# Optimization experiments

Measured on AMD Instinct MI355X. Metric: run time of the kernel, lower is better.

Reference implementation:

```python
import jax, jax.numpy as jnp
import numpy as np

B, S, D, H = 4, 1024, 1024, 16
HD = D // H  # head dim = 64
SCALE = 1.0 / float(np.sqrt(HD))
W_INIT = 0.02


def setup_inputs() -> dict:
    key = jax.random.key(0)
    ks = jax.random.split(key, 8)
    f = lambda k, shape: jax.random.normal(k, shape, dtype=jnp.float32)
    return {
        "q": f(ks[0], (B, S, D)),
        "k": f(ks[1], (B, S, D)),
        "v": f(ks[2], (B, S, D)),
        "Wq": f(ks[3], (D, D)) * W_INIT, "bq": jnp.zeros((D,), jnp.float32),
        "Wk": f(ks[4], (D, D)) * W_INIT, "bk": jnp.zeros((D,), jnp.float32),
        "Wv": f(ks[5], (D, D)) * W_INIT, "bv": jnp.zeros((D,), jnp.float32),
        "Wo": f(ks[6], (D, D)) * W_INIT, "bo": jnp.zeros((D,), jnp.float32),
    }


def _split_heads(x):
    # [B, S, D] -> [B, H, S, HD]
    return x.reshape(B, S, H, HD).transpose(0, 2, 1, 3)


def reference(q, k, v, Wq, bq, Wk, bk, Wv, bv, Wo, bo):
    # linear input projections (torch Linear: x @ W.T + b)
    qh = _split_heads(q @ Wq.T + bq) * SCALE
    kh = _split_heads(k @ Wk.T + bk)
    vh = _split_heads(v @ Wv.T + bv)
    # scaled dot-product attention, full score matrix as in the source
    scores = jnp.einsum("bhqd,bhkd->bhqk", qh, kh)  # [B,H,S,S]
    weights = jax.nn.softmax(scores, axis=-1)
    ctx = jnp.einsum("bhqk,bhkd->bhqd", weights, vh)  # [B,H,S,HD]
    ctx = ctx.transpose(0, 2, 1, 3).reshape(B, S, D)
    # output projection (dropout=0, activation=None -> identity)
    return ctx @ Wo.T + bo
```

## Files before the change

kernel.cpp:

```cpp
#include <hip/hip_runtime.h>
#include <hip/hip_bf16.h>

typedef __attribute__((ext_vector_type(8))) short short8;
typedef __attribute__((ext_vector_type(4))) float f32x4;

static __device__ __forceinline__ short f2bf(float x) {
    __hip_bfloat16 h(x);
    return __builtin_bit_cast(short, h);
}

static __device__ __forceinline__ void gload16(const void* g, void* l) {
    auto* gp = reinterpret_cast<const __attribute__((address_space(1))) unsigned*>(
        reinterpret_cast<uintptr_t>(g));
    auto* lp = reinterpret_cast<__attribute__((address_space(3))) unsigned*>(
        reinterpret_cast<uintptr_t>(l));
    __builtin_amdgcn_global_load_lds(gp, lp, 16, 0, 0);
}

template <int CTRL>
static __device__ __forceinline__ float dppf(float v) {
    return __builtin_bit_cast(float,
        __builtin_amdgcn_mov_dpp(__builtin_bit_cast(int, v), CTRL, 0xF, 0xF, true));
}
static __device__ __forceinline__ float red16_max(float v) {
    v = fmaxf(v, dppf<0xB1>(v));
    v = fmaxf(v, dppf<0x4E>(v));
    v = fmaxf(v, dppf<0x141>(v));
    v = fmaxf(v, dppf<0x140>(v));
    return v;
}
static __device__ __forceinline__ float red16_sum(float v) {
    v += dppf<0xB1>(v);
    v += dppf<0x4E>(v);
    v += dppf<0x141>(v);
    v += dppf<0x140>(v);
    return v;
}

__global__ __launch_bounds__(256) void convert_w3(
    const float* __restrict__ Wq, const float* __restrict__ Wk,
    const float* __restrict__ Wv, short* __restrict__ dst)
{
    const size_t e = ((size_t)blockIdx.x * 256 + threadIdx.x) * 8;
    const int seg = (int)(e >> 20);
    const float* src = (seg == 0) ? Wq : (seg == 1) ? Wk : Wv;
    const size_t off = e & 1048575;
    float4 f0 = *(const float4*)(src + off);
    float4 f1 = *(const float4*)(src + off + 4);
    short8 o;
    o[0] = f2bf(f0.x); o[1] = f2bf(f0.y); o[2] = f2bf(f0.z); o[3] = f2bf(f0.w);
    o[4] = f2bf(f1.x); o[5] = f2bf(f1.y); o[6] = f2bf(f1.z); o[7] = f2bf(f1.w);
    *(short8*)(dst + e) = o;
}

__global__ __launch_bounds__(256) void convert_w1(
    const float* __restrict__ W, short* __restrict__ dst)
{
    const size_t e = ((size_t)blockIdx.x * 256 + threadIdx.x) * 8;
    float4 f0 = *(const float4*)(W + e);
    float4 f1 = *(const float4*)(W + e + 4);
    short8 o;
    o[0] = f2bf(f0.x); o[1] = f2bf(f0.y); o[2] = f2bf(f0.z); o[3] = f2bf(f0.w);
    o[4] = f2bf(f1.x); o[5] = f2bf(f1.y); o[6] = f2bf(f1.z); o[7] = f2bf(f1.w);
    *(short8*)(dst + e) = o;
}

__global__ __launch_bounds__(256) void proj_qkv_kernel(
    const float* __restrict__ q, const float* __restrict__ k, const float* __restrict__ v,
    const short* __restrict__ wbf,
    const float* __restrict__ bq, const float* __restrict__ bk, const float* __restrict__ bv,
    short* __restrict__ qh, short* __restrict__ kh, short* __restrict__ vt)
{
    const int z = blockIdx.z;
    const float* A    = (z == 0) ? q  : (z == 1) ? k  : v;
    const short* W    = wbf + (size_t)z * 1048576;
    const float* bias = (z == 0) ? bq : (z == 1) ? bk : bv;

    __shared__ __align__(16) short As[2][128 * 32];
    __shared__ __align__(16) short Bs[2][128 * 32];

    const int tid = threadIdx.x;
    const int lane = tid & 63;
    const int w = tid >> 6;
    const int wr = w >> 1, wc = w & 1;
    const int row0 = blockIdx.x * 128;
    const int col0 = blockIdx.y * 128;
    const int fr = lane & 15;
    const int g = lane >> 4;
    const int fk = g * 8;

    const int brow = lane >> 2;
    const int bch  = (lane & 3) * 8;
    const int arow = tid >> 2;
    const int ach  = (tid & 3) * 8;

    f32x4 acc[4][4] = {};
    float4 pfA[2][2];

    #pragma unroll
    for (int i = 0; i < 2; ++i) {
        const int r0 = w * 32 + i * 16;
        gload16(W + (size_t)(col0 + r0 + brow) * 1024 + bch, &Bs[0][r0 * 32]);
    }
    #pragma unroll
    for (int p = 0; p < 2; ++p) {
        const int r = p * 64 + arow;
        const float* s = A + (size_t)(row0 + r) * 1024 + ach;
        float4 f0 = *(const float4*)s, f1 = *(const float4*)(s + 4);
        short8 o;
        o[0] = f2bf(f0.x); o[1] = f2bf(f0.y); o[2] = f2bf(f0.z); o[3] = f2bf(f0.w);
        o[4] = f2bf(f1.x); o[5] = f2bf(f1.y); o[6] = f2bf(f1.z); o[7] = f2bf(f1.w);
        *(short8*)&As[0][r * 32 + ach] = o;
    }
    __syncthreads();

    for (int t = 0; t < 32; ++t) {
        const int cur = t & 1, nxt = cur ^ 1;
        if (t < 31) {
            const int k1 = (t + 1) * 32;
            #pragma unroll
            for (int i = 0; i < 2; ++i) {
                const int r0 = w * 32 + i * 16;
                gload16(W + (size_t)(col0 + r0 + brow) * 1024 + k1 + bch, &Bs[nxt][r0 * 32]);
            }
            #pragma unroll
            for (int p = 0; p < 2; ++p) {
                const float* s = A + (size_t)(row0 + p * 64 + arow) * 1024 + k1 + ach;
                pfA[p][0] = *(const float4*)s;
                pfA[p][1] = *(const float4*)(s + 4);
            }
        }
        short8 aF[4], bF[4];
        #pragma unroll
        for (int m = 0; m < 4; ++m) aF[m] = *(const short8*)&As[cur][(wr * 64 + m * 16 + fr) * 32 + fk];
        #pragma unroll
        for (int n = 0; n < 4; ++n) bF[n] = *(const short8*)&Bs[cur][(wc * 64 + n * 16 + fr) * 32 + fk];
        if (z == 2) {
            #pragma unroll
            for (int m = 0; m < 4; ++m)
                #pragma unroll
                for (int n = 0; n < 4; ++n)
                    acc[m][n] = __builtin_amdgcn_mfma_f32_16x16x32_bf16(bF[n], aF[m], acc[m][n], 0, 0, 0);
        } else {
            #pragma unroll
            for (int m = 0; m < 4; ++m)
                #pragma unroll
                for (int n = 0; n < 4; ++n)
                    acc[m][n] = __builtin_amdgcn_mfma_f32_16x16x32_bf16(aF[m], bF[n], acc[m][n], 0, 0, 0);
        }
        if (t < 31) {
            #pragma unroll
            for (int p = 0; p < 2; ++p) {
                float4 f0 = pfA[p][0], f1 = pfA[p][1];
                short8 o;
                o[0] = f2bf(f0.x); o[1] = f2bf(f0.y); o[2] = f2bf(f0.z); o[3] = f2bf(f0.w);
                o[4] = f2bf(f1.x); o[5] = f2bf(f1.y); o[6] = f2bf(f1.z); o[7] = f2bf(f1.w);
                *(short8*)&As[nxt][(p * 64 + arow) * 32 + ach] = o;
            }
        }
        __syncthreads();
    }

    const int gg = lane >> 4;
    if (z == 2) {
        #pragma unroll
        for (int n = 0; n < 4; ++n) {
            #pragma unroll
            for (int i = 0; i < 4; ++i) {
                const int c = col0 + wc * 64 + n * 16 + gg * 4 + i;
                const int h = c >> 6, hd = c & 63;
                const float bb = bias[c];
                #pragma unroll
                for (int m = 0; m < 4; ++m) {
                    const int r = row0 + wr * 64 + m * 16 + fr;
                    const int b = r >> 10, s = r & 1023;
                    vt[(((size_t)(b * 16 + h) * 64 + hd) << 10) + s] = f2bf(acc[m][n][i] + bb);
                }
            }
        }
    } else {
        short* out = (z == 0) ? qh : kh;
        const float scale = (z == 0) ? 0.125f : 1.0f;
        #pragma unroll
        for (int n = 0; n < 4; ++n) {
            const int c = col0 + wc * 64 + n * 16 + fr;
            const int h = c >> 6, hd = c & 63;
            const float bb = bias[c];
            #pragma unroll
            for (int m = 0; m < 4; ++m) {
                #pragma unroll
                for (int i = 0; i < 4; ++i) {
                    const int r = row0 + wr * 64 + m * 16 + gg * 4 + i;
                    const int b = r >> 10, s = r & 1023;
                    out[(((size_t)(b * 16 + h) * 1024 + s) << 6) + hd] =
                        f2bf((acc[m][n][i] + bb) * scale);
                }
            }
        }
    }
}

__global__ __launch_bounds__(256) void proj_o_kernel(
    const short* __restrict__ ctx, const short* __restrict__ wo,
    const float* __restrict__ bo, float* __restrict__ out)
{
    __shared__ __align__(16) short As[2][128 * 32];
    __shared__ __align__(16) short Bs[2][64 * 32];

    const int tid = threadIdx.x;
    const int lane = tid & 63;
    const int w = tid >> 6;
    const int row0 = blockIdx.x * 128;
    const int col0 = blockIdx.y * 64;
    const int fr = lane & 15;
    const int g = lane >> 4;
    const int fk = g * 8;
    const int brow = lane >> 2;
    const int bch  = (lane & 3) * 8;

    f32x4 acc[2][4] = {};

    #pragma unroll
    for (int i = 0; i < 2; ++i) {
        const int r0 = w * 32 + i * 16;
        gload16(ctx + (size_t)(row0 + r0 + brow) * 1024 + bch, &As[0][r0 * 32]);
    }
    gload16(wo + (size_t)(col0 + w * 16 + brow) * 1024 + bch, &Bs[0][w * 16 * 32]);
    __syncthreads();

    for (int t = 0; t < 32; ++t) {
        const int cur = t & 1, nxt = cur ^ 1;
        if (t < 31) {
            const int k1 = (t + 1) * 32;
            #pragma unroll
            for (int i = 0; i < 2; ++i) {
                const int r0 = w * 32 + i * 16;
                gload16(ctx + (size_t)(row0 + r0 + brow) * 1024 + k1 + bch, &As[nxt][r0 * 32]);
            }
            gload16(wo + (size_t)(col0 + w * 16 + brow) * 1024 + k1 + bch, &Bs[nxt][w * 16 * 32]);
        }
        short8 aF[2], bF[4];
        #pragma unroll
        for (int m = 0; m < 2; ++m)
            aF[m] = *(const short8*)&As[cur][(w * 32 + m * 16 + fr) * 32 + fk];
        #pragma unroll
        for (int n = 0; n < 4; ++n)
            bF[n] = *(const short8*)&Bs[cur][(n * 16 + fr) * 32 + fk];
        #pragma unroll
        for (int m = 0; m < 2; ++m)
            #pragma unroll
            for (int n = 0; n < 4; ++n)
                acc[m][n] = __builtin_amdgcn_mfma_f32_16x16x32_bf16(aF[m], bF[n], acc[m][n], 0, 0, 0);
        __syncthreads();
    }

    #pragma unroll
    for (int n = 0; n < 4; ++n) {
        const int c = col0 + n * 16 + fr;
        const float bb = bo[c];
        #pragma unroll
        for (int m = 0; m < 2; ++m) {
            #pragma unroll
            for (int i = 0; i < 4; ++i) {
                const int r = row0 + w * 32 + m * 16 + g * 4 + i;
                out[(size_t)r * 1024 + c] = acc[m][n][i] + bb;
            }
        }
    }
}

__global__ __launch_bounds__(256) void attn_kernel(
    const short* __restrict__ qh, const short* __restrict__ kh,
    const short* __restrict__ vt, short* __restrict__ ctx)
{
    const int d = blockIdx.x;
    const int xcd = d & 7;
    const int s2 = d >> 3;
    const int bh = xcd * 8 + (s2 >> 3);
    const int qb = s2 & 7;
    const int b = bh >> 4, h = bh & 15;
    const int q0 = qb * 128;
    const short* Qh  = qh + (size_t)bh * 65536;
    const short* Kh  = kh + (size_t)bh * 65536;
    const short* Vth = vt + (size_t)bh * 65536;

    __shared__ __align__(16) short Ks[2][64 * 64];
    __shared__ __align__(16) short Vs[2][64 * 64];
    __shared__ __align__(16) short Pb[4][2][16 * 68];

    const int tid = threadIdx.x;
    const int lane = tid & 63;
    const int w = tid >> 6;
    const int fr = lane & 15;
    const int g = lane >> 4;
    const int fk = g * 8;
    const int srow = lane >> 3;
    const int sch  = ((lane & 7) ^ srow) * 8;

    short8 qF[2][2];
    #pragma unroll
    for (int m = 0; m < 2; ++m)
        #pragma unroll
        for (int j = 0; j < 2; ++j)
            qF[m][j] = *(const short8*)(Qh + (q0 + w * 32 + m * 16 + fr) * 64 + j * 32 + fk);

    float mi[2][4], li[2][4];
    f32x4 o[2][4] = {};
    #pragma unroll
    for (int m = 0; m < 2; ++m)
        #pragma unroll
        for (int i = 0; i < 4; ++i) { mi[m][i] = -3.0e38f; li[m][i] = 0.0f; }

    #pragma unroll
    for (int i = 0; i < 2; ++i) {
        const int r0 = w * 16 + i * 8;
        gload16(Kh + (size_t)(r0 + srow) * 64 + sch, &Ks[0][r0 * 64]);
        gload16(Vth + (size_t)(r0 + srow) * 1024 + sch, &Vs[0][r0 * 64]);
    }
    __syncthreads();

    for (int kt = 0; kt < 16; ++kt) {
        const int cur = kt & 1;
        if (kt < 15) {
            const int kv1 = (kt + 1) * 64;
            #pragma unroll
            for (int i = 0; i < 2; ++i) {
                const int r0 = w * 16 + i * 8;
                gload16(Kh + (size_t)(kv1 + r0 + srow) * 64 + sch, &Ks[cur ^ 1][r0 * 64]);
                gload16(Vth + (size_t)(r0 + srow) * 1024 + kv1 + sch, &Vs[cur ^ 1][r0 * 64]);
            }
        }

        f32x4 sc[2][4] = {};
        #pragma unroll
        for (int n = 0; n < 4; ++n) {
            const int r = n * 16 + fr;
            #pragma unroll
            for (int j = 0; j < 2; ++j) {
                short8 kF = *(const short8*)&Ks[cur][r * 64 + (((j * 4 + g) ^ (fr & 7)) * 8)];
                #pragma unroll
                for (int m = 0; m < 2; ++m)
                    sc[m][n] = __builtin_amdgcn_mfma_f32_16x16x32_bf16(qF[m][j], kF, sc[m][n], 0, 0, 0);
            }
        }

        #pragma unroll
        for (int m = 0; m < 2; ++m) {
            #pragma unroll
            for (int i = 0; i < 4; ++i) {
                float t0 = fmaxf(fmaxf(sc[m][0][i], sc[m][1][i]),
                                 fmaxf(sc[m][2][i], sc[m][3][i]));
                const float tm = red16_max(t0);
                const float mn = fmaxf(mi[m][i], tm);
                const float al = __expf(mi[m][i] - mn);
                mi[m][i] = mn;
                float s0 = 0.0f;
                #pragma unroll
                for (int n = 0; n < 4; ++n) {
                    const float pv = __expf(sc[m][n][i] - mn);
                    s0 += pv;
                    Pb[w][m][(g * 4 + i) * 68 + n * 16 + fr] = f2bf(pv);
                }
                li[m][i] = li[m][i] * al + red16_sum(s0);
                #pragma unroll
                for (int n = 0; n < 4; ++n) o[m][n][i] *= al;
            }
        }

        #pragma unroll
        for (int half = 0; half < 2; ++half) {
            short8 pF[2];
            #pragma unroll
            for (int m = 0; m < 2; ++m)
                pF[m] = *(const short8*)&Pb[w][m][fr * 68 + half * 32 + fk];
            #pragma unroll
            for (int n = 0; n < 4; ++n) {
                short8 vF = *(const short8*)&Vs[cur][(n * 16 + fr) * 64 + (((half * 4 + g) ^ (fr & 7)) * 8)];
                #pragma unroll
                for (int m = 0; m < 2; ++m)
                    o[m][n] = __builtin_amdgcn_mfma_f32_16x16x32_bf16(pF[m], vF, o[m][n], 0, 0, 0);
            }
        }
        __syncthreads();
    }

    #pragma unroll
    for (int m = 0; m < 2; ++m) {
        float inv[4];
        #pragma unroll
        for (int i = 0; i < 4; ++i) inv[i] = 1.0f / li[m][i];
        #pragma unroll
        for (int n = 0; n < 4; ++n)
            #pragma unroll
            for (int i = 0; i < 4; ++i) {
                const int s = q0 + w * 32 + m * 16 + g * 4 + i;
                ctx[(size_t)(b * 1024 + s) * 1024 + h * 64 + n * 16 + fr] = f2bf(o[m][n][i] * inv[i]);
            }
    }
}

extern "C" void kernel_launch(void* const* d_in, const int* in_sizes, int n_in,
                              void* d_out, int out_size, void* d_ws, size_t ws_size,
                              hipStream_t stream) {
    const float* q  = (const float*)d_in[0];
    const float* k  = (const float*)d_in[1];
    const float* v  = (const float*)d_in[2];
    const float* Wq = (const float*)d_in[3];
    const float* bq = (const float*)d_in[4];
    const float* Wk = (const float*)d_in[5];
    const float* bk = (const float*)d_in[6];
    const float* Wv = (const float*)d_in[7];
    const float* bv = (const float*)d_in[8];
    const float* Wo = (const float*)d_in[9];
    const float* bo = (const float*)d_in[10];

    char* ws = (char*)d_ws;
    const size_t SZ = (size_t)4096 * 1024 * 2;
    short* qh  = (short*)(ws);
    short* kh  = (short*)(ws + SZ);
    short* vt  = (short*)(ws + 2 * SZ);
    short* ctx = (short*)(ws + 3 * SZ);
    short* wscratch = (short*)d_out;

    convert_w3<<<1536, 256, 0, stream>>>(Wq, Wk, Wv, wscratch);
    proj_qkv_kernel<<<dim3(32, 8, 3), 256, 0, stream>>>(
        q, k, v, wscratch, bq, bk, bv, qh, kh, vt);
    attn_kernel<<<512, 256, 0, stream>>>(qh, kh, vt, ctx);
    convert_w1<<<512, 256, 0, stream>>>(Wo, qh);
    proj_o_kernel<<<dim3(32, 16), 256, 0, stream>>>(ctx, qh, bo, (float*)d_out);
}
```

Before: 249.1 us.

## Pre-convert activations to bf16, use 64-wide K tiles, enlarge output tiles, add setprio

Input activations and all four weights are converted to bf16 in one kernel, and the QKV projection loads bf16 tiles straight into LDS with global_load_lds instead of converting fp32 in registers. Both projection GEMMs now use single-buffered 128x64 K tiles with two MFMA sub-steps, replacing double-buffered 32-wide tiles. The output projection moves to 128x128 tiles, and the attention MFMA sections get s_setprio hints. The extra conversion pass writes and rereads the activations, and dropping double buffering exposes load latency.

```diff
diff --git a/kernel.cpp b/kernel.cpp
--- a/kernel.cpp
+++ b/kernel.cpp
@@ -37,47 +37,49 @@
     return v;
 }
 
-__global__ __launch_bounds__(256) void convert_w3(
+__global__ __launch_bounds__(256) void convert_all(
+    const float* __restrict__ q, const float* __restrict__ k, const float* __restrict__ v,
     const float* __restrict__ Wq, const float* __restrict__ Wk,
-    const float* __restrict__ Wv, short* __restrict__ dst)
+    const float* __restrict__ Wv, const float* __restrict__ Wo,
+    short* __restrict__ abf_q, short* __restrict__ abf_k, short* __restrict__ abf_v,
+    short* __restrict__ wbf)
 {
-    const size_t e = ((size_t)blockIdx.x * 256 + threadIdx.x) * 8;
-    const int seg = (int)(e >> 20);
-    const float* src = (seg == 0) ? Wq : (seg == 1) ? Wk : Wv;
-    const size_t off = e & 1048575;
+    const int blk = blockIdx.x;
+    const float* src;
+    short* dst;
+    size_t off;
+    if (blk < 6144) {
+        const int seg = blk >> 11;
+        src = (seg == 0) ? q : (seg == 1) ? k : v;
+        dst = (seg == 0) ? abf_q : (seg == 1) ? abf_k : abf_v;
+        off = ((size_t)(blk & 2047) * 256 + threadIdx.x) * 8;
+    } else {
+        const int wseg = (blk - 6144) >> 9;
+        src = (wseg == 0) ? Wq : (wseg == 1) ? Wk : (wseg == 2) ? Wv : Wo;
+        dst = wbf + (size_t)wseg * 1048576;
+        off = ((size_t)((blk - 6144) & 511) * 256 + threadIdx.x) * 8;
+    }
     float4 f0 = *(const float4*)(src + off);
     float4 f1 = *(const float4*)(src + off + 4);
     short8 o;
     o[0] = f2bf(f0.x); o[1] = f2bf(f0.y); o[2] = f2bf(f0.z); o[3] = f2bf(f0.w);
     o[4] = f2bf(f1.x); o[5] = f2bf(f1.y); o[6] = f2bf(f1.z); o[7] = f2bf(f1.w);
-    *(short8*)(dst + e) = o;
-}
-
-__global__ __launch_bounds__(256) void convert_w1(
-    const float* __restrict__ W, short* __restrict__ dst)
-{
-    const size_t e = ((size_t)blockIdx.x * 256 + threadIdx.x) * 8;
-    float4 f0 = *(const float4*)(W + e);
-    float4 f1 = *(const float4*)(W + e + 4);
-    short8 o;
-    o[0] = f2bf(f0.x); o[1] = f2bf(f0.y); o[2] = f2bf(f0.z); o[3] = f2bf(f0.w);
-    o[4] = f2bf(f1.x); o[5] = f2bf(f1.y); o[6] = f2bf(f1.z); o[7] = f2bf(f1.w);
-    *(short8*)(dst + e) = o;
+    *(short8*)(dst + off) = o;
 }
 
 __global__ __launch_bounds__(256) void proj_qkv_kernel(
-    const float* __restrict__ q, const float* __restrict__ k, const float* __restrict__ v,
-    const short* __restrict__ wbf,
+    const short* __restrict__ abf_q, const short* __restrict__ abf_k,
+    const short* __restrict__ abf_v, const short* __restrict__ wbf,
     const float* __restrict__ bq, const float* __restrict__ bk, const float* __restrict__ bv,
     short* __restrict__ qh, short* __restrict__ kh, short* __restrict__ vt)
 {
     const int z = blockIdx.z;
-    const float* A    = (z == 0) ? q  : (z == 1) ? k  : v;
+    const short* A    = (z == 0) ? abf_q : (z == 1) ? abf_k : abf_v;
     const short* W    = wbf + (size_t)z * 1048576;
     const float* bias = (z == 0) ? bq : (z == 1) ? bk : bv;
 
-    __shared__ __align__(16) short As[2][128 * 32];
-    __shared__ __align__(16) short Bs[2][128 * 32];
+    __shared__ __align__(16) short As[128 * 64];
+    __shared__ __align__(16) short Bs[128 * 64];
 
     const int tid = threadIdx.x;
     const int lane = tid & 63;
@@ -88,86 +90,52 @@
     const int fr = lane & 15;
     const int g = lane >> 4;
     const int fk = g * 8;
-
-    const int brow = lane >> 2;
-    const int bch  = (lane & 3) * 8;
-    const int arow = tid >> 2;
-    const int ach  = (tid & 3) * 8;
+    const int srow = lane >> 3;
+    const int sch  = (lane & 7) * 8;
 
     f32x4 acc[4][4] = {};
-    float4 pfA[2][2];
-
-    #pragma unroll
-    for (int i = 0; i < 2; ++i) {
-        const int r0 = w * 32 + i * 16;
-        gload16(W + (size_t)(col0 + r0 + brow) * 1024 + bch, &Bs[0][r0 * 32]);
-    }
-    #pragma unroll
-    for (int p = 0; p < 2; ++p) {
-        const int r = p * 64 + arow;
-        const float* s = A + (size_t)(row0 + r) * 1024 + ach;
-        float4 f0 = *(const float4*)s, f1 = *(const float4*)(s + 4);
-        short8 o;
-        o[0] = f2bf(f0.x); o[1] = f2bf(f0.y); o[2] = f2bf(f0.z); o[3] = f2bf(f0.w);
-        o[4] = f2bf(f1.x); o[5] = f2bf(f1.y); o[6] = f2bf(f1.z); o[7] = f2bf(f1.w);
-        *(short8*)&As[0][r * 32 + ach] = o;
-    }
-    __syncthreads();
-
-    for (int t = 0; t < 32; ++t) {
-        const int cur = t & 1, nxt = cur ^ 1;
-        if (t < 31) {
-            const int k1 = (t + 1) * 32;
-            #pragma unroll
-            for (int i = 0; i < 2; ++i) {
-                const int r0 = w * 32 + i * 16;
-                gload16(W + (size_t)(col0 + r0 + brow) * 1024 + k1 + bch, &Bs[nxt][r0 * 32]);
-            }
-            #pragma unroll
-            for (int p = 0; p < 2; ++p) {
-                const float* s = A + (size_t)(row0 + p * 64 + arow) * 1024 + k1 + ach;
-                pfA[p][0] = *(const float4*)s;
-                pfA[p][1] = *(const float4*)(s + 4);
-            }
-        }
-        short8 aF[4], bF[4];
-        #pragma unroll
-        for (int m = 0; m < 4; ++m) aF[m] = *(const short8*)&As[cur][(wr * 64 + m * 16 + fr) * 32 + fk];
-        #pragma unroll
-        for (int n = 0; n < 4; ++n) bF[n] = *(const short8*)&Bs[cur][(wc * 64 + n * 16 + fr) * 32 + fk];
-        if (z == 2) {
+
+    for (int t = 0; t < 16; ++t) {
+        const int k0 = t * 64;
+        #pragma unroll
+        for (int i = 0; i < 4; ++i) {
+            const int r0 = w * 32 + i * 8;
+            gload16(A + (size_t)(row0 + r0 + srow) * 1024 + k0 + sch, &As[r0 * 64]);
+            gload16(W + (size_t)(col0 + r0 + srow) * 1024 + k0 + sch, &Bs[r0 * 64]);
+        }
+        __syncthreads();
+        #pragma unroll
+        for (int kk = 0; kk < 2; ++kk) {
+            short8 aF[4], bF[4];
             #pragma unroll
             for (int m = 0; m < 4; ++m)
-                #pragma unroll
-                for (int n = 0; n < 4; ++n)
-                    acc[m][n] = __builtin_amdgcn_mfma_f32_16x16x32_bf16(bF[n], aF[m], acc[m][n], 0, 0, 0);
-        } else {
-            #pragma unroll
-            for (int m = 0; m < 4; ++m)
-                #pragma unroll
-                for (int n = 0; n < 4; ++n)
-                    acc[m][n] = __builtin_amdgcn_mfma_f32_16x16x32_bf16(aF[m], bF[n], acc[m][n], 0, 0, 0);
-        }
-        if (t < 31) {
-            #pragma unroll
-            for (int p = 0; p < 2; ++p) {
-                float4 f0 = pfA[p][0], f1 = pfA[p][1];
-                short8 o;
-                o[0] = f2bf(f0.x); o[1] = f2bf(f0.y); o[2] = f2bf(f0.z); o[3] = f2bf(f0.w);
-                o[4] = f2bf(f1.x); o[5] = f2bf(f1.y); o[6] = f2bf(f1.z); o[7] = f2bf(f1.w);
-                *(short8*)&As[nxt][(p * 64 + arow) * 32 + ach] = o;
+                aF[m] = *(const short8*)&As[(wr * 64 + m * 16 + fr) * 64 + kk * 32 + fk];
+            #pragma unroll
+            for (int n = 0; n < 4; ++n)
+                bF[n] = *(const short8*)&Bs[(wc * 64 + n * 16 + fr) * 64 + kk * 32 + fk];
+            if (z == 2) {
+                #pragma unroll
+                for (int m = 0; m < 4; ++m)
+                    #pragma unroll
+                    for (int n = 0; n < 4; ++n)
+                        acc[m][n] = __builtin_amdgcn_mfma_f32_16x16x32_bf16(bF[n], aF[m], acc[m][n], 0, 0, 0);
+            } else {
+                #pragma unroll
+                for (int m = 0; m < 4; ++m)
+                    #pragma unroll
+                    for (int n = 0; n < 4; ++n)
+                        acc[m][n] = __builtin_amdgcn_mfma_f32_16x16x32_bf16(aF[m], bF[n], acc[m][n], 0, 0, 0);
             }
         }
         __syncthreads();
     }
 
-    const int gg = lane >> 4;
     if (z == 2) {
         #pragma unroll
         for (int n = 0; n < 4; ++n) {
             #pragma unroll
             for (int i = 0; i < 4; ++i) {
-                const int c = col0 + wc * 64 + n * 16 + gg * 4 + i;
+                const int c = col0 + wc * 64 + n * 16 + g * 4 + i;
                 const int h = c >> 6, hd = c & 63;
                 const float bb = bias[c];
                 #pragma unroll
@@ -190,7 +158,7 @@
             for (int m = 0; m < 4; ++m) {
                 #pragma unroll
                 for (int i = 0; i < 4; ++i) {
-                    const int r = row0 + wr * 64 + m * 16 + gg * 4 + i;
+                    const int r = row0 + wr * 64 + m * 16 + g * 4 + i;
                     const int b = r >> 10, s = r & 1023;
                     out[(((size_t)(b * 16 + h) * 1024 + s) << 6) + hd] =
                         f2bf((acc[m][n][i] + bb) * scale);
@@ -204,65 +172,59 @@
     const short* __restrict__ ctx, const short* __restrict__ wo,
     const float* __restrict__ bo, float* __restrict__ out)
 {
-    __shared__ __align__(16) short As[2][128 * 32];
-    __shared__ __align__(16) short Bs[2][64 * 32];
+    __shared__ __align__(16) short As[128 * 64];
+    __shared__ __align__(16) short Bs[128 * 64];
 
     const int tid = threadIdx.x;
     const int lane = tid & 63;
     const int w = tid >> 6;
+    const int wr = w >> 1, wc = w & 1;
     const int row0 = blockIdx.x * 128;
-    const int col0 = blockIdx.y * 64;
+    const int col0 = blockIdx.y * 128;
     const int fr = lane & 15;
     const int g = lane >> 4;
     const int fk = g * 8;
-    const int brow = lane >> 2;
-    const int bch  = (lane & 3) * 8;
-
-    f32x4 acc[2][4] = {};
-
-    #pragma unroll
-    for (int i = 0; i < 2; ++i) {
-        const int r0 = w * 32 + i * 16;
-        gload16(ctx + (size_t)(row0 + r0 + brow) * 1024 + bch, &As[0][r0 * 32]);
-    }
-    gload16(wo + (size_t)(col0 + w * 16 + brow) * 1024 + bch, &Bs[0][w * 16 * 32]);
-    __syncthreads();
-
-    for (int t = 0; t < 32; ++t) {
-        const int cur = t & 1, nxt = cur ^ 1;
-        if (t < 31) {
-            const int k1 = (t + 1) * 32;
-            #pragma unroll
-            for (int i = 0; i < 2; ++i) {
-                const int r0 = w * 32 + i * 16;
-                gload16(ctx + (size_t)(row0 + r0 + brow) * 1024 + k1 + bch, &As[nxt][r0 * 32]);
-            }
-            gload16(wo + (size_t)(col0 + w * 16 + brow) * 1024 + k1 + bch, &Bs[nxt][w * 16 * 32]);
-        }
-        short8 aF[2], bF[4];
-        #pragma unroll
-        for (int m = 0; m < 2; ++m)
-            aF[m] = *(const short8*)&As[cur][(w * 32 + m * 16 + fr) * 32 + fk];
-        #pragma unroll
-        for (int n = 0; n < 4; ++n)
-            bF[n] = *(const short8*)&Bs[cur][(n * 16 + fr) * 32 + fk];
-        #pragma unroll
-        for (int m = 0; m < 2; ++m)
+    const int srow = lane >> 3;
+    const int sch  = (lane & 7) * 8;
+
+    f32x4 acc[4][4] = {};
+
+    for (int t = 0; t < 16; ++t) {
+        const int k0 = t * 64;
+        #pragma unroll
+        for (int i = 0; i < 4; ++i) {
+            const int r0 = w * 32 + i * 8;
+            gload16(ctx + (size_t)(row0 + r0 + srow) * 1024 + k0 + sch, &As[r0 * 64]);
+            gload16(wo + (size_t)(col0 + r0 + srow) * 1024 + k0 + sch, &Bs[r0 * 64]);
+        }
+        __syncthreads();
+        #pragma unroll
+        for (int kk = 0; kk < 2; ++kk) {
+            short8 aF[4], bF[4];
+            #pragma unroll
+            for (int m = 0; m < 4; ++m)
+                aF[m] = *(const short8*)&As[(wr * 64 + m * 16 + fr) * 64 + kk * 32 + fk];
             #pragma unroll
             for (int n = 0; n < 4; ++n)
-                acc[m][n] = __builtin_amdgcn_mfma_f32_16x16x32_bf16(aF[m], bF[n], acc[m][n], 0, 0, 0);
+                bF[n] = *(const short8*)&Bs[(wc * 64 + n * 16 + fr) * 64 + kk * 32 + fk];
+            #pragma unroll
+            for (int m = 0; m < 4; ++m)
+                #pragma unroll
+                for (int n = 0; n < 4; ++n)
+                    acc[m][n] = __builtin_amdgcn_mfma_f32_16x16x32_bf16(aF[m], bF[n], acc[m][n], 0, 0, 0);
+        }
         __syncthreads();
     }
 
     #pragma unroll
     for (int n = 0; n < 4; ++n) {
-        const int c = col0 + n * 16 + fr;
+        const int c = col0 + wc * 64 + n * 16 + fr;
         const float bb = bo[c];
         #pragma unroll
-        for (int m = 0; m < 2; ++m) {
+        for (int m = 0; m < 4; ++m) {
             #pragma unroll
             for (int i = 0; i < 4; ++i) {
-                const int r = row0 + w * 32 + m * 16 + g * 4 + i;
+                const int r = row0 + wr * 64 + m * 16 + g * 4 + i;
                 out[(size_t)r * 1024 + c] = acc[m][n][i] + bb;
             }
         }
@@ -332,6 +294,7 @@
         }
 
         f32x4 sc[2][4] = {};
+        __builtin_amdgcn_s_setprio(1);
         #pragma unroll
         for (int n = 0; n < 4; ++n) {
             const int r = n * 16 + fr;
@@ -343,6 +306,7 @@
                     sc[m][n] = __builtin_amdgcn_mfma_f32_16x16x32_bf16(qF[m][j], kF, sc[m][n], 0, 0, 0);
             }
         }
+        __builtin_amdgcn_s_setprio(0);
 
         #pragma unroll
         for (int m = 0; m < 2; ++m) {
@@ -367,6 +331,7 @@
             }
         }
 
+        __builtin_amdgcn_s_setprio(1);
         #pragma unroll
         for (int half = 0; half < 2; ++half) {
             short8 pF[2];
@@ -381,6 +346,7 @@
                     o[m][n] = __builtin_amdgcn_mfma_f32_16x16x32_bf16(pF[m], vF, o[m][n], 0, 0, 0);
             }
         }
+        __builtin_amdgcn_s_setprio(0);
         __syncthreads();
     }
 
@@ -416,16 +382,19 @@
 
     char* ws = (char*)d_ws;
     const size_t SZ = (size_t)4096 * 1024 * 2;
-    short* qh  = (short*)(ws);
-    short* kh  = (short*)(ws + SZ);
-    short* vt  = (short*)(ws + 2 * SZ);
-    short* ctx = (short*)(ws + 3 * SZ);
-    short* wscratch = (short*)d_out;
-
-    convert_w3<<<1536, 256, 0, stream>>>(Wq, Wk, Wv, wscratch);
+    short* qh    = (short*)(ws);
+    short* kh    = (short*)(ws + SZ);
+    short* vt    = (short*)(ws + 2 * SZ);
+    short* ctx   = (short*)(ws + 3 * SZ);
+    short* abf_v = (short*)(ws + 4 * SZ);
+    short* wbf   = (short*)(ws + 5 * SZ);
+    short* abf_q = (short*)d_out;
+    short* abf_k = (short*)d_out + 4194304;
+
+    convert_all<<<8192, 256, 0, stream>>>(q, k, v, Wq, Wk, Wv, Wo,
+                                          abf_q, abf_k, abf_v, wbf);
     proj_qkv_kernel<<<dim3(32, 8, 3), 256, 0, stream>>>(
-        q, k, v, wscratch, bq, bk, bv, qh, kh, vt);
+        abf_q, abf_k, abf_v, wbf, bq, bk, bv, qh, kh, vt);
     attn_kernel<<<512, 256, 0, stream>>>(qh, kh, vt, ctx);
-    convert_w1<<<512, 256, 0, stream>>>(Wo, qh);
-    proj_o_kernel<<<dim3(32, 16), 256, 0, stream>>>(ctx, qh, bo, (float*)d_out);
-}
+    proj_o_kernel<<<dim3(32, 8), 256, 0, stream>>>(ctx, wbf + 3 * 1048576, bo, (float*)d_out);
+}
```

New measurement: 231.4 us. -7.1%, faster.
